# Optimization experiments

Hardware: AMD Instinct MI355X
Metric: run time of the kernel (lower is better)

Reference implementation:

```python
import jax, jax.numpy as jnp
import numpy as np
from jax import lax

LATENT_DIM = 512
TOKEN_DIM = 256
KERNEL = 5
STRIDE = 5


def setup_inputs() -> dict:
    key = jax.random.key(0)
    ks = jax.random.split(key, 8)
    B, L, S = 8, 1024, 10240
    s = lambda fan_in: 1.0 / np.sqrt(fan_in)
    return {
        "latents": jax.random.normal(ks[0], (B, L, LATENT_DIM), dtype=jnp.float32),
        "tokens": jax.random.normal(ks[1], (B, S, TOKEN_DIM), dtype=jnp.float32),
        # nn.Linear weights, stored as (out, in) like torch
        "W_lat": jax.random.uniform(ks[2], (LATENT_DIM, LATENT_DIM), jnp.float32, -s(LATENT_DIM), s(LATENT_DIM)),
        "W_tok": jax.random.uniform(ks[3], (LATENT_DIM, LATENT_DIM), jnp.float32, -s(LATENT_DIM), s(LATENT_DIM)),
        "W_vlat": jax.random.uniform(ks[4], (LATENT_DIM, LATENT_DIM), jnp.float32, -s(LATENT_DIM), s(LATENT_DIM)),
        "W_vtok": jax.random.uniform(ks[5], (LATENT_DIM, LATENT_DIM), jnp.float32, -s(LATENT_DIM), s(LATENT_DIM)),
        # Conv1d weight (out_ch, in_ch, k) and bias
        "conv_w": jax.random.uniform(ks[6], (LATENT_DIM, TOKEN_DIM, KERNEL), jnp.float32, -s(TOKEN_DIM * KERNEL), s(TOKEN_DIM * KERNEL)),
        "conv_b": jax.random.uniform(ks[7], (LATENT_DIM,), jnp.float32, -s(TOKEN_DIM * KERNEL), s(TOKEN_DIM * KERNEL)),
    }


def reference(latents, tokens, W_lat, W_tok, W_vlat, W_vtok, conv_w, conv_b):
    # Conv1d: (B,S,token_dim) -> (B,S//5,latent_dim)
    tok = lax.conv_general_dilated(
        tokens.transpose(0, 2, 1), conv_w, window_strides=(STRIDE,),
        padding="VALID", dimension_numbers=("NCH", "OIH", "NCH"))
    tok = (tok + conv_b[None, :, None]).transpose(0, 2, 1)  # (B, S', D)

    R_lat = jnp.einsum("bld,ed->ble", latents, W_lat)
    R_tok = jnp.einsum("bsd,ed->bse", tok, W_tok)
    V_lat = jnp.einsum("bld,ed->ble", latents, W_vlat)
    V_tok = jnp.einsum("bsd,ed->bse", tok, W_vtok)

    # shared score matrix, used for both row-wise and column-wise softmax
    A = jnp.einsum("ble,bse->bls", R_lat, R_tok) / jnp.sqrt(jnp.float32(LATENT_DIM))
    delta_lat = jnp.einsum("bls,bse->ble", jax.nn.softmax(A, axis=-1), V_tok)
    delta_tok = jnp.einsum("bls,ble->bse", jax.nn.softmax(A, axis=1), V_lat)

    updated_latents = latents + delta_lat
    updated_tokens = tok + delta_tok
    output = jnp.concatenate([updated_latents, updated_tokens], axis=1)
    return (updated_latents, updated_tokens, output)
```

## Files before the change

### kernel.cpp

```cpp
#include <hip/hip_runtime.h>
#include <math.h>

#define SCALEF 0.044194173824159216f

typedef __attribute__((ext_vector_type(8))) short bf16x8;
typedef __attribute__((ext_vector_type(4))) float f32x4;

static __device__ __forceinline__ unsigned short f2bf(float f) {
    union { float f; unsigned int i; } v; v.f = f;
    return (unsigned short)((v.i + 0x7fffu + ((v.i >> 16) & 1u)) >> 16);
}
static __device__ __forceinline__ float bf2f(unsigned short h) {
    union { unsigned int i; float f; } v; v.i = ((unsigned int)h) << 16;
    return v.f;
}
static __device__ __forceinline__ void gload16(const void* g, void* l) {
    __builtin_amdgcn_global_load_lds(
        (const __attribute__((address_space(1))) unsigned int*)g,
        (__attribute__((address_space(3))) unsigned int*)l, 16, 0, 0);
}
static __device__ __forceinline__ int swz(int l, int n) {
    return (l & 7) * (n >> 3) + (l >> 3);
}

__global__ __launch_bounds__(256) void cvt_tl(const float4* __restrict__ tok,
                                              const float4* __restrict__ lat,
                                              ushort4* __restrict__ tokd,
                                              ushort4* __restrict__ latd) {
    long t = blockIdx.x * 256L + threadIdx.x;
    #pragma unroll
    for (int k = 0; k < 5; ++k) {
        long i = t + k * 1048576L;
        float4 f = tok[i];
        ushort4 u; u.x = f2bf(f.x); u.y = f2bf(f.y); u.z = f2bf(f.z); u.w = f2bf(f.w);
        tokd[i] = u;
    }
    {
        float4 f = lat[t];
        ushort4 u; u.x = f2bf(f.x); u.y = f2bf(f.y); u.z = f2bf(f.z); u.w = f2bf(f.w);
        latd[t] = u;
    }
}

__global__ __launch_bounds__(256) void prep_rest(
    const float* __restrict__ wl, const float* __restrict__ wt,
    const float4* __restrict__ wvl, const float4* __restrict__ wvt,
    const float* __restrict__ cw,
    ushort4* __restrict__ wlT, ushort4* __restrict__ wtT,
    ushort4* __restrict__ wvlb, ushort4* __restrict__ wvtb,
    unsigned int* __restrict__ wpb)
{
    const long NW = 65536, NCV = 327680;
    for (long i = blockIdx.x * 256L + threadIdx.x; i < 4 * NW + NCV;
         i += gridDim.x * 256L) {
        long r = i;
        if (r < 2 * NW) {
            const float* src = (r < NW) ? wl : wt;
            ushort4* dst = (r < NW) ? wlT : wtT;
            long u = (r < NW) ? r : r - NW;
            int a = (int)(u >> 7), e4 = (int)(u & 127);
            ushort4 o;
            o.x = f2bf(src[(e4 * 4 + 0) * 512 + a]);
            o.y = f2bf(src[(e4 * 4 + 1) * 512 + a]);
            o.z = f2bf(src[(e4 * 4 + 2) * 512 + a]);
            o.w = f2bf(src[(e4 * 4 + 3) * 512 + a]);
            dst[a * 128 + e4] = o;
            continue;
        }
        r -= 2 * NW;
        const float4* s; ushort4* d;
        if (r < NW) { s = wvl; d = wvlb; }
        else if ((r -= NW) < NW) { s = wvt; d = wvtb; }
        else {
            r -= NW;
            long e = r / 640, rr = r % 640, k = rr >> 7, c2 = rr & 127;
            unsigned int lo = f2bf(cw[e * 1280 + (2 * c2) * 5 + k]);
            unsigned int hi = f2bf(cw[e * 1280 + (2 * c2 + 1) * 5 + k]);
            wpb[r] = lo | (hi << 16);
            continue;
        }
        float4 f = s[r];
        ushort4 u; u.x = f2bf(f.x); u.y = f2bf(f.y); u.z = f2bf(f.z); u.w = f2bf(f.w);
        d[r] = u;
    }
}

template<int RL>
static __device__ __forceinline__ void sm_body(unsigned short* __restrict__ rowp,
                                               float* __restrict__ redm,
                                               float* __restrict__ reds) {
    constexpr int U = RL / 512;
    unsigned int* p = (unsigned int*)rowp;
    const int t = threadIdx.x, lane = t & 63, wid = t >> 6;
    unsigned int u[U];
    float v[2 * U];
    #pragma unroll
    for (int i = 0; i < U; ++i) u[i] = p[t + (i << 8)];
    #pragma unroll
    for (int i = 0; i < U; ++i) {
        v[2 * i]     = bf2f((unsigned short)(u[i] & 0xffffu));
        v[2 * i + 1] = bf2f((unsigned short)(u[i] >> 16));
    }
    float m = -INFINITY;
    #pragma unroll
    for (int i = 0; i < 2 * U; ++i) m = fmaxf(m, v[i]);
    #pragma unroll
    for (int k = 1; k < 64; k <<= 1) m = fmaxf(m, __shfl_xor(m, k));
    if (lane == 0) redm[wid] = m;
    __syncthreads();
    m = fmaxf(fmaxf(redm[0], redm[1]), fmaxf(redm[2], redm[3]));
    float s = 0.f, e[2 * U];
    #pragma unroll
    for (int i = 0; i < 2 * U; ++i) { e[i] = __expf(v[i] - m); s += e[i]; }
    #pragma unroll
    for (int k = 1; k < 64; k <<= 1) s += __shfl_xor(s, k);
    if (lane == 0) reds[wid] = s;
    __syncthreads();
    s = reds[0] + reds[1] + reds[2] + reds[3];
    float inv = 1.f / s;
    #pragma unroll
    for (int i = 0; i < U; ++i) {
        unsigned int lo = f2bf(e[2 * i] * inv);
        unsigned int hi = f2bf(e[2 * i + 1] * inv);
        p[t + (i << 8)] = lo | (hi << 16);
    }
}

__global__ __launch_bounds__(256) void softmax_both(unsigned short* __restrict__ S,
                                                    unsigned short* __restrict__ ST) {
    __shared__ float redm[4], reds[4];
    long b = blockIdx.x;
    if (b < 8192) sm_body<2048>(S + b * 2048L, redm, reds);
    else          sm_body<1024>(ST + (b - 8192) * 1024L, redm, reds);
}

template<int AMODE, int EPI>
static __device__ __forceinline__ void mm_body(
    char* __restrict__ smc, int bx, int by, int z,
    const unsigned short* __restrict__ A, const unsigned short* __restrict__ B,
    long bsA, long bsB, int lda, int ldb, int K,
    unsigned short* __restrict__ Cb, long bsCb,
    float* __restrict__ C0, long bsC0, float* __restrict__ C1, long bsC1,
    const void* __restrict__ basep, long bsBase, int ldc, float scale)
{
    const int t = threadIdx.x, lane = t & 63, wid = t >> 6;
    const int m0 = by << 7, n0 = bx << 7;
    const unsigned short* Ab = A + (long)z * bsA;
    const unsigned short* Bb = B + (long)z * bsB;

    const int rA0 = wid * 16 + (lane >> 2);
    const int rA1 = rA0 + 64;
    const int cs0 = (lane & 3) ^ ((rA0 >> 1) & 3);
    const int cs1 = (lane & 3) ^ ((rA1 >> 1) & 3);

    long aoff0, aoff1;
    if (AMODE == 0) {
        aoff0 = (long)(m0 + rA0) * lda + cs0 * 8;
        aoff1 = (long)(m0 + rA1) * lda + cs1 * 8;
    } else {
        int ma = m0 + rA0, mb = m0 + rA1;
        aoff0 = (long)(ma >> 11) * 2621440 + (long)(ma & 2047) * 1280 + cs0 * 8;
        aoff1 = (long)(mb >> 11) * 2621440 + (long)(mb & 2047) * 1280 + cs1 * 8;
    }
    const long boff0 = (long)(n0 + rA0) * ldb + cs0 * 8;
    const long boff1 = (long)(n0 + rA1) * ldb + cs1 * 8;

    const int dA0 = (wid << 10), dA1 = ((wid + 4) << 10);
    const int dB0 = 8192 + (wid << 10), dB1 = 8192 + ((wid + 4) << 10);

    const int wr = wid >> 1, wc = wid & 1;
    const int l15 = lane & 15, cslot = lane >> 4;
    int offA[4], offB[4];
    #pragma unroll
    for (int i = 0; i < 4; ++i) {
        int r = wr * 64 + i * 16 + l15;
        offA[i] = r * 64 + ((cslot ^ ((r >> 1) & 3)) << 4);
        int rb = wc * 64 + i * 16 + l15;
        offB[i] = 8192 + rb * 64 + ((cslot ^ ((rb >> 1) & 3)) << 4);
    }

    f32x4 acc[4][4];
    #pragma unroll
    for (int i = 0; i < 4; ++i)
        #pragma unroll
        for (int j = 0; j < 4; ++j)
            acc[i][j] = (f32x4)(0.f);

#define STAGE(p, ktv) do {                                   \
        int kb_ = (ktv);                                     \
        int bo_ = (p) * 16384;                               \
        gload16(Ab + aoff0 + kb_, smc + bo_ + dA0);          \
        gload16(Ab + aoff1 + kb_, smc + bo_ + dA1);          \
        gload16(Bb + boff0 + kb_, smc + bo_ + dB0);          \
        gload16(Bb + boff1 + kb_, smc + bo_ + dB1);          \
    } while (0)

    const int nt = K >> 5;
    STAGE(0, 0);
    STAGE(1, 32);
    int cur = 0;
    for (int it = 0; it < nt; ++it) {
        if (it + 2 < nt) {
            int nx2 = (cur >= 1) ? cur - 1 : 2;
            STAGE(nx2, (it + 2) << 5);
            asm volatile("s_waitcnt vmcnt(8)" ::: "memory");
        } else if (it + 1 < nt) {
            asm volatile("s_waitcnt vmcnt(4)" ::: "memory");
        } else {
            asm volatile("s_waitcnt vmcnt(0)" ::: "memory");
        }
        __builtin_amdgcn_s_barrier();
        const char* base = smc + cur * 16384;
        bf16x8 af[4], bfr[4];
        #pragma unroll
        for (int i = 0; i < 4; ++i) af[i]  = *(const bf16x8*)(base + offA[i]);
        #pragma unroll
        for (int i = 0; i < 4; ++i) bfr[i] = *(const bf16x8*)(base + offB[i]);
        #pragma unroll
        for (int i = 0; i < 4; ++i)
            #pragma unroll
            for (int j = 0; j < 4; ++j)
                acc[i][j] = __builtin_amdgcn_mfma_f32_16x16x32_bf16(af[i], bfr[j], acc[i][j], 0, 0, 0);
        asm volatile("s_waitcnt lgkmcnt(0)" ::: "memory");
        __builtin_amdgcn_s_barrier();
        cur = (cur + 1 == 3) ? 0 : cur + 1;
    }
#undef STAGE

    const int colb = n0 + wc * 64 + l15;
    const int rowb = m0 + wr * 64 + cslot * 4;
    if (EPI == 4) {
        unsigned short* STp = (unsigned short*)C0;
        #pragma unroll
        for (int i = 0; i < 4; ++i) {
            #pragma unroll
            for (int j = 0; j < 4; ++j) {
                int n = colb + j * 16;
                int mb = rowb + i * 16;
                float v0 = acc[i][j][0] * scale, v1 = acc[i][j][1] * scale;
                float v2 = acc[i][j][2] * scale, v3 = acc[i][j][3] * scale;
                unsigned short b0 = f2bf(v0), b1 = f2bf(v1), b2 = f2bf(v2), b3 = f2bf(v3);
                unsigned short* sp = Cb + (long)z * bsCb + (long)mb * ldc + n;
                sp[0] = b0; sp[ldc] = b1; sp[2 * ldc] = b2; sp[3 * ldc] = b3;
                ushort4 st4; st4.x = b0; st4.y = b1; st4.z = b2; st4.w = b3;
                *(ushort4*)(STp + (long)z * bsC0 + (long)n * bsC1 + mb) = st4;
            }
        }
        return;
    }
    #pragma unroll
    for (int i = 0; i < 4; ++i) {
        #pragma unroll
        for (int j = 0; j < 4; ++j) {
            int n = colb + j * 16;
            #pragma unroll
            for (int q = 0; q < 4; ++q) {
                int m = rowb + i * 16 + q;
                float v = acc[i][j][q];
                if (EPI == 0) {
                    Cb[(long)z * bsCb + (long)m * ldc + n] = f2bf(v * scale);
                } else if (EPI == 1) {
                    v += ((const float*)basep)[n];
                    Cb[(long)m * ldc + n] = f2bf(v);
                } else if (EPI == 2) {
                    float bv = ((const float*)basep)[(long)z * bsBase + (long)m * ldc + n];
                    float o = bv + v;
                    C0[(long)z * bsC0 + (long)m * ldc + n] = o;
                    C1[(long)z * bsC1 + (long)m * ldc + n] = o;
                } else {
                    float bv = bf2f(((const unsigned short*)basep)[(long)z * bsBase + (long)m * ldc + n]);
                    float o = bv + v;
                    C0[(long)z * bsC0 + (long)m * ldc + n] = o;
                    C1[(long)z * bsC1 + (long)m * ldc + n] = o;
                }
            }
        }
    }
}

__global__ __launch_bounds__(256) void gemm_g1(
    const unsigned short* __restrict__ tknb, const unsigned short* __restrict__ wpb,
    const float* __restrict__ conv_b, unsigned short* __restrict__ tokb,
    const unsigned short* __restrict__ latb,
    const unsigned short* __restrict__ wvlb, unsigned short* __restrict__ vlT,
    const unsigned short* __restrict__ wtT, const unsigned short* __restrict__ wlT,
    unsigned short* __restrict__ Mt)
{
    __shared__ unsigned short sm[24576];
    char* smc = (char*)sm;
    const int bid = blockIdx.x;
    if (bid < 512) {
        int l = swz(bid, 512);
        mm_body<1, 1>(smc, l & 3, l >> 2, 0, tknb, wpb, 0, 0, 1280, 1280, 1280,
                      tokb, 0, nullptr, 0, nullptr, 0, conv_b, 0, 512, 1.f);
    } else if (bid < 768) {
        int l = swz(bid - 768 + 256, 256);
        mm_body<0, 0>(smc, l & 7, (l >> 3) & 3, l >> 5, wvlb, latb, 0, 524288,
                      512, 512, 512, vlT, 524288, nullptr, 0, nullptr, 0,
                      nullptr, 0, 1024, 1.f);
    } else {
        int l = bid - 768;
        mm_body<0, 0>(smc, l & 3, l >> 2, 0, wtT, wlT, 0, 0, 512, 512, 512,
                      Mt, 0, nullptr, 0, nullptr, 0, nullptr, 0, 512, 1.f);
    }
}

__global__ __launch_bounds__(256) void gemm_g2(
    const unsigned short* __restrict__ tokb,
    const unsigned short* __restrict__ wvtb, unsigned short* __restrict__ vtT,
    const unsigned short* __restrict__ latb, const unsigned short* __restrict__ Mt,
    unsigned short* __restrict__ P)
{
    __shared__ unsigned short sm[24576];
    char* smc = (char*)sm;
    const int bid = blockIdx.x;
    if (bid < 512) {
        int l = swz(bid, 512);
        mm_body<0, 0>(smc, l & 15, (l >> 4) & 3, l >> 6, wvtb, tokb, 0, 1048576,
                      512, 512, 512, vtT, 1048576, nullptr, 0, nullptr, 0,
                      nullptr, 0, 2048, 1.f);
    } else {
        int l = swz(bid - 512, 256);
        mm_body<0, 0>(smc, l & 3, l >> 2, 0, latb, Mt, 0, 0, 512, 512, 512,
                      P, 0, nullptr, 0, nullptr, 0, nullptr, 0, 512, 1.f);
    }
}

__global__ __launch_bounds__(256) void gemm_sc(
    const unsigned short* __restrict__ P, const unsigned short* __restrict__ tokb,
    unsigned short* __restrict__ S, unsigned short* __restrict__ ST)
{
    __shared__ unsigned short sm[24576];
    int l = swz((int)blockIdx.x, 1024);
    mm_body<0, 4>((char*)sm, l & 15, (l >> 4) & 7, l >> 7,
                  P, tokb, 524288, 1048576, 512, 512, 512,
                  S, 2097152, (float*)ST, 2097152, nullptr, 1024,
                  nullptr, 0, 2048, SCALEF);
}

__global__ __launch_bounds__(256) void gemm_g3(
    const unsigned short* __restrict__ S, const unsigned short* __restrict__ ST,
    const unsigned short* __restrict__ vlT, const unsigned short* __restrict__ vtT,
    const float* __restrict__ latents, const unsigned short* __restrict__ tokb,
    float* __restrict__ out)
{
    __shared__ unsigned short sm[24576];
    char* smc = (char*)sm;
    const int bid = blockIdx.x;
    if (bid < 256) {
        int l = swz(bid, 256);
        mm_body<0, 2>(smc, l & 3, (l >> 2) & 7, l >> 5, S, vtT, 2097152, 1048576,
                      2048, 2048, 2048, nullptr, 0,
                      out, 524288, out + 12582912, 1572864,
                      latents, 524288, 512, 1.f);
    } else {
        int l = swz(bid - 256, 512);
        mm_body<0, 3>(smc, l & 3, (l >> 2) & 15, l >> 6, ST, vlT, 2097152, 524288,
                      1024, 1024, 1024, nullptr, 0,
                      out + 4194304, 1048576, out + 12582912 + 524288, 1572864,
                      tokb, 1048576, 512, 1.f);
    }
}

extern "C" void kernel_launch(void* const* d_in, const int* in_sizes, int n_in,
                              void* d_out, int out_size, void* d_ws, size_t ws_size,
                              hipStream_t stream)
{
    const float* latents = (const float*)d_in[0];
    const float* tokens  = (const float*)d_in[1];
    const float* W_lat   = (const float*)d_in[2];
    const float* W_tok   = (const float*)d_in[3];
    const float* W_vlat  = (const float*)d_in[4];
    const float* W_vtok  = (const float*)d_in[5];
    const float* conv_w  = (const float*)d_in[6];
    const float* conv_b  = (const float*)d_in[7];
    float* out = (float*)d_out;
    char* ws = (char*)d_ws;

    unsigned short* S    = (unsigned short*)(ws);
    unsigned short* ST   = (unsigned short*)(ws + 33554432);
    unsigned short* tokb = (unsigned short*)(ws + 67108864);
    unsigned short* latb = (unsigned short*)(ws + 83886080);
    unsigned short* P    = (unsigned short*)(ws + 92274688);
    unsigned short* Mt   = (unsigned short*)(ws + 100663296);
    unsigned short* vlT  = (unsigned short*)(ws + 117440512);
    unsigned short* vtT  = (unsigned short*)(ws + 125829120);
    unsigned short* wpb  = (unsigned short*)(ws + 142606336);
    unsigned short* wlT  = (unsigned short*)(ws + 143917056);
    unsigned short* wtT  = (unsigned short*)(ws + 144441344);
    unsigned short* wvlb = (unsigned short*)(ws + 144965632);
    unsigned short* wvtb = (unsigned short*)(ws + 145489920);
    unsigned short* tknb = (unsigned short*)(out + 12582912);

    cvt_tl<<<4096, 256, 0, stream>>>((const float4*)tokens, (const float4*)latents,
                                     (ushort4*)tknb, (ushort4*)latb);
    prep_rest<<<512, 256, 0, stream>>>(
        W_lat, W_tok, (const float4*)W_vlat, (const float4*)W_vtok, conv_w,
        (ushort4*)wlT, (ushort4*)wtT, (ushort4*)wvlb, (ushort4*)wvtb,
        (unsigned int*)wpb);

    gemm_g1<<<784, 256, 0, stream>>>(tknb, wpb, conv_b, tokb,
                                     latb, wvlb, vlT, wtT, wlT, Mt);

    gemm_g2<<<768, 256, 0, stream>>>(tokb, wvtb, vtT, latb, Mt, P);

    gemm_sc<<<1024, 256, 0, stream>>>(P, tokb, S, ST);

    softmax_both<<<24576, 256, 0, stream>>>(S, ST);

    gemm_g3<<<768, 256, 0, stream>>>(S, ST, vlT, vtT, latents, tokb, out);
}
```

Baseline: 227.6 us.

## Fuse fp32-to-bf16 token conversion into conv GEMM A-operand loading

Drops the separate pass that converted the tokens tensor to bf16. The conv GEMM now reads fp32 tokens directly into registers one stage ahead, converts them to bf16, and writes them into the LDS ring while the B operand still uses async global-to-LDS loads. This saves a full write and re-read of a roughly 40MB bf16 tokens copy. In exchange the A loads go through registers, and the convert and LDS stores sit in the pipelined main loop with changed vmcnt accounting. The g1 block swizzle index for the second branch is also simplified.

Result: slower. 253.7 us (+11.5%).

```diff
diff --git a/kernel.cpp b/kernel.cpp
--- a/kernel.cpp
+++ b/kernel.cpp
@@ -23,22 +23,15 @@
     return (l & 7) * (n >> 3) + (l >> 3);
 }
 
-__global__ __launch_bounds__(256) void cvt_tl(const float4* __restrict__ tok,
-                                              const float4* __restrict__ lat,
-                                              ushort4* __restrict__ tokd,
-                                              ushort4* __restrict__ latd) {
+__global__ __launch_bounds__(256) void cvt_lat(const float4* __restrict__ lat,
+                                               ushort4* __restrict__ latd) {
     long t = blockIdx.x * 256L + threadIdx.x;
     #pragma unroll
-    for (int k = 0; k < 5; ++k) {
-        long i = t + k * 1048576L;
-        float4 f = tok[i];
+    for (int k = 0; k < 2; ++k) {
+        long i = t + k * 524288L;
+        float4 f = lat[i];
         ushort4 u; u.x = f2bf(f.x); u.y = f2bf(f.y); u.z = f2bf(f.z); u.w = f2bf(f.w);
-        tokd[i] = u;
-    }
-    {
-        float4 f = lat[t];
-        ushort4 u; u.x = f2bf(f.x); u.y = f2bf(f.y); u.z = f2bf(f.z); u.w = f2bf(f.w);
-        latd[t] = u;
+        latd[i] = u;
     }
 }
 
@@ -186,6 +179,24 @@
         for (int j = 0; j < 4; ++j)
             acc[i][j] = (f32x4)(0.f);
 
+#define COMPUTE(c) do {                                                        \
+        const char* base_ = smc + (c) * 16384;                                 \
+        bf16x8 af[4], bfr[4];                                                  \
+        _Pragma("unroll")                                                      \
+        for (int i = 0; i < 4; ++i) af[i]  = *(const bf16x8*)(base_ + offA[i]);\
+        _Pragma("unroll")                                                      \
+        for (int i = 0; i < 4; ++i) bfr[i] = *(const bf16x8*)(base_ + offB[i]);\
+        _Pragma("unroll")                                                      \
+        for (int i = 0; i < 4; ++i)                                            \
+            _Pragma("unroll")                                                  \
+            for (int j = 0; j < 4; ++j)                                        \
+                acc[i][j] = __builtin_amdgcn_mfma_f32_16x16x32_bf16(           \
+                    af[i], bfr[j], acc[i][j], 0, 0, 0);                        \
+    } while (0)
+
+    const int nt = K >> 5;
+
+    if constexpr (AMODE != 2) {
 #define STAGE(p, ktv) do {                                   \
         int kb_ = (ktv);                                     \
         int bo_ = (p) * 16384;                               \
@@ -194,38 +205,101 @@
         gload16(Bb + boff0 + kb_, smc + bo_ + dB0);          \
         gload16(Bb + boff1 + kb_, smc + bo_ + dB1);          \
     } while (0)
-
-    const int nt = K >> 5;
-    STAGE(0, 0);
-    STAGE(1, 32);
-    int cur = 0;
-    for (int it = 0; it < nt; ++it) {
-        if (it + 2 < nt) {
-            int nx2 = (cur >= 1) ? cur - 1 : 2;
-            STAGE(nx2, (it + 2) << 5);
-            asm volatile("s_waitcnt vmcnt(8)" ::: "memory");
-        } else if (it + 1 < nt) {
-            asm volatile("s_waitcnt vmcnt(4)" ::: "memory");
-        } else {
-            asm volatile("s_waitcnt vmcnt(0)" ::: "memory");
-        }
-        __builtin_amdgcn_s_barrier();
-        const char* base = smc + cur * 16384;
-        bf16x8 af[4], bfr[4];
-        #pragma unroll
-        for (int i = 0; i < 4; ++i) af[i]  = *(const bf16x8*)(base + offA[i]);
-        #pragma unroll
-        for (int i = 0; i < 4; ++i) bfr[i] = *(const bf16x8*)(base + offB[i]);
-        #pragma unroll
-        for (int i = 0; i < 4; ++i)
-            #pragma unroll
-            for (int j = 0; j < 4; ++j)
-                acc[i][j] = __builtin_amdgcn_mfma_f32_16x16x32_bf16(af[i], bfr[j], acc[i][j], 0, 0, 0);
+        STAGE(0, 0);
+        STAGE(1, 32);
+        int cur = 0;
+        for (int it = 0; it < nt; ++it) {
+            if (it + 2 < nt) {
+                int nx2 = (cur >= 1) ? cur - 1 : 2;
+                STAGE(nx2, (it + 2) << 5);
+                asm volatile("s_waitcnt vmcnt(8)" ::: "memory");
+            } else if (it + 1 < nt) {
+                asm volatile("s_waitcnt vmcnt(4)" ::: "memory");
+            } else {
+                asm volatile("s_waitcnt vmcnt(0)" ::: "memory");
+            }
+            __builtin_amdgcn_s_barrier();
+            COMPUTE(cur);
+            asm volatile("s_waitcnt lgkmcnt(0)" ::: "memory");
+            __builtin_amdgcn_s_barrier();
+            cur = (cur + 1 == 3) ? 0 : cur + 1;
+        }
+#undef STAGE
+    } else {
+        const float* Af = (const float*)A;
+        float4 eL0, eH0, eL1, eH1;
+        float4 oL0, oH0, oL1, oH1;
+#define AISS(L0, H0, L1, H1, ktv) do {                                 \
+        const float4* p0_ = (const float4*)(Af + aoff0 + (ktv));       \
+        const float4* p1_ = (const float4*)(Af + aoff1 + (ktv));       \
+        L0 = p0_[0]; H0 = p0_[1]; L1 = p1_[0]; H1 = p1_[1]; } while (0)
+#define PKU(a, b) (((unsigned int)f2bf(a)) | (((unsigned int)f2bf(b)) << 16))
+#define CVTW(L0, H0, L1, H1, bufp) do {                                \
+        int bo_ = (bufp) * 16384;                                      \
+        uint4 w_;                                                      \
+        w_.x = PKU(L0.x, L0.y); w_.y = PKU(L0.z, L0.w);                \
+        w_.z = PKU(H0.x, H0.y); w_.w = PKU(H0.z, H0.w);                \
+        *(uint4*)(smc + bo_ + dA0 + (lane << 4)) = w_;                 \
+        w_.x = PKU(L1.x, L1.y); w_.y = PKU(L1.z, L1.w);                \
+        w_.z = PKU(H1.x, H1.y); w_.w = PKU(H1.z, H1.w);                \
+        *(uint4*)(smc + bo_ + dA1 + (lane << 4)) = w_; } while (0)
+#define BSTG(p, ktv) do {                                              \
+        int bo_ = (p) * 16384;                                         \
+        gload16(Bb + boff0 + (ktv), smc + bo_ + dB0);                  \
+        gload16(Bb + boff1 + (ktv), smc + bo_ + dB1); } while (0)
+        AISS(eL0, eH0, eL1, eH1, 0);  BSTG(0, 0);
+        AISS(oL0, oH0, oL1, oH1, 32); BSTG(1, 32);
+        CVTW(eL0, eH0, eL1, eH1, 0);
         asm volatile("s_waitcnt lgkmcnt(0)" ::: "memory");
-        __builtin_amdgcn_s_barrier();
-        cur = (cur + 1 == 3) ? 0 : cur + 1;
-    }
-#undef STAGE
+        int cur = 0;
+        for (int it = 0; it < nt; it += 2) {
+            {
+                if (it + 2 < nt) {
+                    int nx2 = (cur >= 1) ? cur - 1 : 2;
+                    AISS(eL0, eH0, eL1, eH1, (it + 2) << 5);
+                    BSTG(nx2, (it + 2) << 5);
+                    asm volatile("s_waitcnt vmcnt(8)" ::: "memory");
+                } else if (it + 1 < nt) {
+                    asm volatile("s_waitcnt vmcnt(6)" ::: "memory");
+                } else {
+                    asm volatile("s_waitcnt vmcnt(0)" ::: "memory");
+                }
+                __builtin_amdgcn_s_barrier();
+                COMPUTE(cur);
+                int nb = (cur + 1 == 3) ? 0 : cur + 1;
+                if (it + 1 < nt) CVTW(oL0, oH0, oL1, oH1, nb);
+                asm volatile("s_waitcnt lgkmcnt(0)" ::: "memory");
+                __builtin_amdgcn_s_barrier();
+                cur = nb;
+            }
+            {
+                int jt = it + 1;
+                if (jt >= nt) break;
+                if (jt + 2 < nt) {
+                    int nx2 = (cur >= 1) ? cur - 1 : 2;
+                    AISS(oL0, oH0, oL1, oH1, (jt + 2) << 5);
+                    BSTG(nx2, (jt + 2) << 5);
+                    asm volatile("s_waitcnt vmcnt(8)" ::: "memory");
+                } else if (jt + 1 < nt) {
+                    asm volatile("s_waitcnt vmcnt(6)" ::: "memory");
+                } else {
+                    asm volatile("s_waitcnt vmcnt(0)" ::: "memory");
+                }
+                __builtin_amdgcn_s_barrier();
+                COMPUTE(cur);
+                int nb = (cur + 1 == 3) ? 0 : cur + 1;
+                if (jt + 1 < nt) CVTW(eL0, eH0, eL1, eH1, nb);
+                asm volatile("s_waitcnt lgkmcnt(0)" ::: "memory");
+                __builtin_amdgcn_s_barrier();
+                cur = nb;
+            }
+        }
+#undef AISS
+#undef PKU
+#undef CVTW
+#undef BSTG
+    }
+#undef COMPUTE
 
     const int colb = n0 + wc * 64 + l15;
     const int rowb = m0 + wr * 64 + cslot * 4;
@@ -279,7 +353,7 @@
 }
 
 __global__ __launch_bounds__(256) void gemm_g1(
-    const unsigned short* __restrict__ tknb, const unsigned short* __restrict__ wpb,
+    const float* __restrict__ tokens, const unsigned short* __restrict__ wpb,
     const float* __restrict__ conv_b, unsigned short* __restrict__ tokb,
     const unsigned short* __restrict__ latb,
     const unsigned short* __restrict__ wvlb, unsigned short* __restrict__ vlT,
@@ -291,10 +365,11 @@
     const int bid = blockIdx.x;
     if (bid < 512) {
         int l = swz(bid, 512);
-        mm_body<1, 1>(smc, l & 3, l >> 2, 0, tknb, wpb, 0, 0, 1280, 1280, 1280,
+        mm_body<2, 1>(smc, l & 3, l >> 2, 0, (const unsigned short*)tokens, wpb,
+                      0, 0, 1280, 1280, 1280,
                       tokb, 0, nullptr, 0, nullptr, 0, conv_b, 0, 512, 1.f);
     } else if (bid < 768) {
-        int l = swz(bid - 768 + 256, 256);
+        int l = swz(bid - 512, 256);
         mm_body<0, 0>(smc, l & 7, (l >> 3) & 3, l >> 5, wvlb, latb, 0, 524288,
                       512, 512, 512, vlT, 524288, nullptr, 0, nullptr, 0,
                       nullptr, 0, 1024, 1.f);
@@ -390,16 +465,14 @@
     unsigned short* wtT  = (unsigned short*)(ws + 144441344);
     unsigned short* wvlb = (unsigned short*)(ws + 144965632);
     unsigned short* wvtb = (unsigned short*)(ws + 145489920);
-    unsigned short* tknb = (unsigned short*)(out + 12582912);
-
-    cvt_tl<<<4096, 256, 0, stream>>>((const float4*)tokens, (const float4*)latents,
-                                     (ushort4*)tknb, (ushort4*)latb);
+
+    cvt_lat<<<2048, 256, 0, stream>>>((const float4*)latents, (ushort4*)latb);
     prep_rest<<<512, 256, 0, stream>>>(
         W_lat, W_tok, (const float4*)W_vlat, (const float4*)W_vtok, conv_w,
         (ushort4*)wlT, (ushort4*)wtT, (ushort4*)wvlb, (ushort4*)wvtb,
         (unsigned int*)wpb);
 
-    gemm_g1<<<784, 256, 0, stream>>>(tknb, wpb, conv_b, tokb,
+    gemm_g1<<<784, 256, 0, stream>>>(tokens, wpb, conv_b, tokb,
                                      latb, wvlb, vlT, wtT, wlT, Mt);
 
     gemm_g2<<<768, 256, 0, stream>>>(tokb, wvtb, vtT, latb, Mt, P);
```
